# Optimization experiments

Hardware: AMD Instinct MI355X
Metric: run time of the kernel (lower is better)

The kernel has to match this reference:

```python
import jax, jax.numpy as jnp
import numpy as np

N_NODES = 100000
N_EDGES = 1600000
IN_DIM = 29
OUT_DIM = 64
BN_EPS = 1e-5


def setup_inputs() -> dict:
    key = jax.random.key(0)
    k1, k2, k3, k4, k5, k6, k7, k8 = jax.random.split(key, 8)
    node = jax.random.normal(k1, (N_NODES, 3), dtype=jnp.float32)
    features = jax.random.normal(k2, (N_NODES, IN_DIM), dtype=jnp.float32)
    edges = jax.random.randint(k3, (N_EDGES, 2), 0, N_NODES, dtype=jnp.int64)
    # Linear(input_dim+3, output_dim, bias=False): weight [out, in+3]
    fan_in = IN_DIM + 3
    weight = jax.random.uniform(k4, (OUT_DIM, fan_in), dtype=jnp.float32,
                                minval=-1.0, maxval=1.0) / np.sqrt(fan_in)
    # BatchNorm1d(output_dim) in eval mode: affine params + running stats
    gamma = jax.random.normal(k5, (OUT_DIM,), dtype=jnp.float32) * 0.1 + 1.0
    beta = jax.random.normal(k6, (OUT_DIM,), dtype=jnp.float32) * 0.1
    running_mean = jax.random.normal(k7, (OUT_DIM,), dtype=jnp.float32) * 0.1
    running_var = jax.random.uniform(k8, (OUT_DIM,), dtype=jnp.float32,
                                     minval=0.5, maxval=1.5)
    return {"node": node, "features": features, "edges": edges,
            "weight": weight, "gamma": gamma, "beta": beta,
            "running_mean": running_mean, "running_var": running_var}


def reference(node, features, edges, weight, gamma, beta, running_mean, running_var):
    dst = edges[:, 0]  # pos_i index (pooling destination)
    src = edges[:, 1]  # pos_j / x_j index
    # gather + concat: msg [E, in+3]
    msg = jnp.concatenate([features[src], node[src] - node[dst]], axis=1)
    # Linear (no bias): [E, out]
    msg = jnp.einsum('ei,oi->eo', msg, weight)
    # BatchNorm1d (eval mode, running stats)
    inv_std = gamma / jnp.sqrt(running_var + BN_EPS)
    msg = (msg - running_mean) * inv_std + beta
    # scatter-max pooling over destination nodes (fixed N segments;
    # torch.unique + scatter_reduce(amax) == segment_max restricted to covered
    # nodes; empty segments filled with 0 matching the zeros init)
    pooled = jax.ops.segment_max(msg, dst, num_segments=N_NODES)
    return jnp.where(jnp.isneginf(pooled), 0.0, pooled)
```

## Files before the change

### kernel.cpp

```cpp
#include <hip/hip_runtime.h>
#include <hip/hip_fp16.h>

#define IN_DIM 29
#define XDIM 32
#define OUT_DIM 64
#define BN_EPS 1e-5f

#define BW      32
#define BW_LOG  5
#define PBLK    256
#define TBLK    2048
#define MAXBUCK 4096
#define SENT    0

#define CS_BPB  32
#define CS_SEG  32

typedef float float4u __attribute__((ext_vector_type(4), aligned(4)));


__global__ __launch_bounds__(256) void fused_tc_kernel(
    const float* __restrict__ features, const float* __restrict__ node,
    const float* __restrict__ weight, const float* __restrict__ gamma,
    const float* __restrict__ rvar, unsigned short* __restrict__ yq,
    const int* __restrict__ edges, int* __restrict__ gHist,
    int n_nodes, int npw, int n_edges, int nbuck, int chunk_c, int cblk)
{
    if ((int)blockIdx.x < cblk) {
        __shared__ int h[MAXBUCK];
        for (int i = threadIdx.x; i < nbuck; i += 256) h[i] = 0;
        __syncthreads();
        const int e0 = blockIdx.x * chunk_c;
        const int e1 = min(e0 + chunk_c, n_edges);
        for (int e = e0 + threadIdx.x; e < e1; e += 256)
            atomicAdd(&h[edges[2*e] >> BW_LOG], 1);
        __syncthreads();
        int* row = gHist + (size_t)blockIdx.x * nbuck;
        for (int i = threadIdx.x; i < nbuck; i += 256) row[i] = h[i];
    } else {
        const int lane = threadIdx.x & 63;
        const int wave = (((int)blockIdx.x - cblk) * 256 + (int)threadIdx.x) >> 6;
        int n0 = wave * npw;
        int n1 = n0 + npw; if (n1 > n_nodes) n1 = n_nodes;

        float w[XDIM];
        const float4* wp = (const float4*)(weight + lane * XDIM);
#pragma unroll
        for (int q = 0; q < 8; ++q) {
            float4 v = wp[q];
            w[4*q+0] = v.x; w[4*q+1] = v.y; w[4*q+2] = v.z; w[4*q+3] = v.w;
        }
        const float a = gamma[lane] * __frsqrt_rn(rvar[lane] + BN_EPS);

        for (int n = n0; n < n1; ++n) {
            const float* f = features + (size_t)n * IN_DIM;
            const float4u* f4 = (const float4u*)f;
            float x[XDIM];
#pragma unroll
            for (int q = 0; q < 7; ++q) {
                float4u v = f4[q];
                x[4*q+0] = v.x; x[4*q+1] = v.y; x[4*q+2] = v.z; x[4*q+3] = v.w;
            }
            x[28] = f[28];
            const float* nd = node + (size_t)n * 3;
            x[29] = nd[0]; x[30] = nd[1]; x[31] = nd[2];
            float acc = 0.0f;
#pragma unroll
            for (int i = 0; i < XDIM; ++i) acc = fmaf(x[i], w[i], acc);
            unsigned short hh = __half_as_ushort(__float2half(acc * a));
            unsigned short enc = (hh & 0x8000) ? (unsigned short)(~hh)
                                               : (unsigned short)(hh | 0x8000);
            yq[(size_t)n * OUT_DIM + lane] = enc;
        }
    }
}

__global__ __launch_bounds__(1024) void colscan_kernel(
    int* __restrict__ gHist, int* __restrict__ bTot,
    int nbuck, int cblk, int R)
{
    const int il = threadIdx.x & (CS_BPB - 1);
    const int s  = threadIdx.x / CS_BPB;
    const int i  = blockIdx.x * CS_BPB + il;
    const int rows = cblk / CS_SEG;
    const int j0 = s * rows;
    __shared__ int sums[CS_SEG][CS_BPB + 1];

    int total = 0;
    if (i < nbuck) {
#pragma unroll 4
        for (int r = 0; r < rows; ++r)
            total += gHist[(size_t)(j0 + r) * nbuck + i];
    }
    sums[s][il] = total;
    __syncthreads();
    if (s == 0) {
        int run = 0;
#pragma unroll
        for (int k = 0; k < CS_SEG; ++k) {
            int t = sums[k][il]; sums[k][il] = run; run += t;
        }
        if (i < nbuck) bTot[i] = run;
    }
    __syncthreads();
    if (i < nbuck) {
        int run = sums[s][il];
        for (int g = j0; g < j0 + rows; g += R) {
            int t[4];
            for (int r = 0; r < R; ++r) t[r] = gHist[(size_t)(g + r) * nbuck + i];
            gHist[(size_t)g * nbuck + i] = run;
            for (int r = 0; r < R; ++r) run += t[r];
        }
    }
}

__global__ __launch_bounds__(256) void scan_b_kernel(int* __restrict__ aux, int nb) {
    const int t = threadIdx.x;
    const int lane = t & 63, wv = t >> 6;
    __shared__ int wsum[4];
    __shared__ int s_run;
    if (t == 0) s_run = 0;
    __syncthreads();
    for (int base = 0; base < nb; base += 256) {
        const int i = base + t;
        int v = (i < nb) ? aux[i] : 0;
        int x = v;
#pragma unroll
        for (int off = 1; off < 64; off <<= 1) {
            int y = __shfl_up(x, off);
            if (lane >= off) x += y;
        }
        if (lane == 63) wsum[wv] = x;
        __syncthreads();
        int wexcl = 0;
        for (int k = 0; k < wv; ++k) wexcl += wsum[k];
        const int run = s_run;
        if (i < nb) aux[i] = run + wexcl + x - v;
        __syncthreads();
        if (t == 255) s_run = run + wexcl + x;
        __syncthreads();
    }
}

__global__ __launch_bounds__(1024) void partition_kernel(
    const int* __restrict__ edges, const int* __restrict__ gHist,
    const int* __restrict__ bOffs,
    int* __restrict__ keys, int n_edges, int nbuck, int chunk_c, int R)
{
    __shared__ int cur[MAXBUCK];
    const int* prow = gHist + (size_t)(R * blockIdx.x) * nbuck;
    for (int i = threadIdx.x; i < nbuck; i += 1024)
        cur[i] = prow[i] + bOffs[i];
    __syncthreads();
    const int chunk_p = R * chunk_c;
    const int e0 = blockIdx.x * chunk_p;
    const int e1 = min(e0 + chunk_p, n_edges);
    for (int e = e0 + threadIdx.x; e < e1; e += 1024) {
        const int dst = edges[2*e], src = edges[2*e+1];
        const int b = dst >> BW_LOG;
        const int pos = atomicAdd(&cur[b], 1);
        keys[pos] = (dst & (BW - 1)) | (src << BW_LOG);
    }
}

__global__ __launch_bounds__(256) void pool_fused_kernel(
    const int* __restrict__ bOffs, const int* __restrict__ keys,
    const unsigned short* __restrict__ yq, const float* __restrict__ node,
    const float* __restrict__ weight, const float* __restrict__ gamma,
    const float* __restrict__ beta, const float* __restrict__ rmean,
    const float* __restrict__ rvar,
    float* __restrict__ out, int n_nodes, int n_edges, int nbuck)
{
    __shared__ int acc[BW * OUT_DIM];
    const int tid = threadIdx.x;
    const int lane = tid & 63, wid = tid >> 6;
    const int b = blockIdx.x;

    {
        int4* p = (int4*)acc;
        for (int i = tid; i < BW * OUT_DIM / 4; i += 256)
            p[i] = make_int4(SENT, SENT, SENT, SENT);
    }
    __syncthreads();

    const int beg = bOffs[b];
    const int end = (b == nbuck - 1) ? n_edges : bOffs[b + 1];

    const int cnt = end - beg;
    const int slice = (cnt + 3) >> 2;
    const int w_beg = beg + wid * slice;
    const int w_end = min(w_beg + slice, end);

    if (w_beg < w_end) {
        const int last = w_end - 1;
        int j = w_beg;
        int kv = keys[min(j + lane, last)];
        while (j < w_end) {
            const int jn = j + 64;
            int kv_n = 0;
            if (jn < w_end) kv_n = keys[min(jn + lane, last)];
            const int m = w_end - j < 64 ? w_end - j : 64;
            const int ng = (m + 7) >> 3;

            unsigned int va[8]; int da[8];
#pragma unroll
            for (int u = 0; u < 8; ++u) {
                const int uu = (u < m) ? u : (m - 1);
                const int key = __builtin_amdgcn_readlane(kv, uu);
                da[u] = key & (BW - 1);
                va[u] = yq[(size_t)((unsigned)key >> BW_LOG) * OUT_DIM + lane];
            }
            for (int g = 0; g < ng; ++g) {
                unsigned int vb[8]; int db[8];
                const bool more = (g + 1 < ng);
                if (more) {
#pragma unroll
                    for (int u = 0; u < 8; ++u) {
                        int uu = (g + 1) * 8 + u; uu = (uu < m) ? uu : (m - 1);
                        const int key = __builtin_amdgcn_readlane(kv, uu);
                        db[u] = key & (BW - 1);
                        vb[u] = yq[(size_t)((unsigned)key >> BW_LOG) * OUT_DIM + lane];
                    }
                }
#pragma unroll
                for (int u = 0; u < 8; ++u)
                    atomicMax(&acc[da[u] * OUT_DIM + lane], (int)va[u]);
                if (more) {
#pragma unroll
                    for (int u = 0; u < 8; ++u) { va[u] = vb[u]; da[u] = db[u]; }
                }
            }
            j = jn; kv = kv_n;
        }
    }
    __syncthreads();

    const float a  = gamma[lane] * __frsqrt_rn(rvar[lane] + BN_EPS);
    const float bp = beta[lane] - rmean[lane] * a;
    const float w29 = weight[lane * XDIM + 29] * a;
    const float w30 = weight[lane * XDIM + 30] * a;
    const float w31 = weight[lane * XDIM + 31] * a;

    for (int d = wid; d < BW; d += 4) {
        const int dg = b * BW + d;
        if (dg >= n_nodes) break;
        const int k = acc[d * OUT_DIM + lane];
        float rr;
        if (k == SENT) {
            rr = 0.0f;
        } else {
            const unsigned short enc = (unsigned short)k;
            const unsigned short h = (enc & 0x8000) ? (unsigned short)(enc ^ 0x8000)
                                                    : (unsigned short)(~enc);
            const float v = __half2float(__ushort_as_half(h));
            const float nx = node[(size_t)dg * 3 + 0];
            const float ny = node[(size_t)dg * 3 + 1];
            const float nz = node[(size_t)dg * 3 + 2];
            rr = v + (bp - (w29 * nx + w30 * ny + w31 * nz));
        }
        out[(size_t)dg * OUT_DIM + lane] = rr;
    }
}

__global__ void init_kernel(int4* __restrict__ out, int total4) {
    int t = blockIdx.x * blockDim.x + threadIdx.x;
    if (t < total4) out[t] = make_int4(INT_MIN, INT_MIN, INT_MIN, INT_MIN);
}

__global__ __launch_bounds__(256) void edge_atomic_kernel(
    const int* __restrict__ edges,
    const float* __restrict__ features, const float* __restrict__ node,
    const float* __restrict__ weight, const float* __restrict__ gamma,
    const float* __restrict__ beta, const float* __restrict__ rmean,
    const float* __restrict__ rvar,
    int* __restrict__ out, int n_edges, int epw)
{
    const int lane = threadIdx.x & 63;
    const int wave = (blockIdx.x * blockDim.x + threadIdx.x) >> 6;
    int e0 = wave * epw, e1 = e0 + epw;
    if (e1 > n_edges) e1 = n_edges;

    float w[XDIM];
    const float4* wp = (const float4*)(weight + lane * XDIM);
#pragma unroll
    for (int q = 0; q < 8; ++q) {
        float4 v = wp[q];
        w[4*q+0] = v.x; w[4*q+1] = v.y; w[4*q+2] = v.z; w[4*q+3] = v.w;
    }
    const float a = gamma[lane] * __frsqrt_rn(rvar[lane] + BN_EPS);
    const float bprime = beta[lane] - rmean[lane] * a;

    for (int e = e0; e < e1; ++e) {
        const int dst = edges[2*e+0], src = edges[2*e+1];
        float x[XDIM];
#pragma unroll
        for (int i = 0; i < IN_DIM; ++i) x[i] = features[(size_t)src * IN_DIM + i];
#pragma unroll
        for (int j = 0; j < 3; ++j)
            x[IN_DIM+j] = node[(size_t)src*3+j] - node[(size_t)dst*3+j];
        float acc = 0.0f;
#pragma unroll
        for (int i = 0; i < XDIM; ++i) acc = fmaf(x[i], w[i], acc);
        float msg = fmaf(acc, a, bprime);
        int bb = __float_as_int(msg);
        int key = (bb < 0) ? (bb ^ 0x7FFFFFFF) : bb;
        atomicMax(out + (size_t)dst * OUT_DIM + lane, key);
    }
}

__global__ void decode_kernel(int* __restrict__ out, int total) {
    int t = blockIdx.x * blockDim.x + threadIdx.x;
    if (t >= total) return;
    int k = out[t];
    float r;
    if (k == INT_MIN) r = 0.0f;
    else { int b = (k < 0) ? (k ^ 0x7FFFFFFF) : k; r = __int_as_float(b); }
    ((float*)out)[t] = r;
}

extern "C" void kernel_launch(void* const* d_in, const int* in_sizes, int n_in,
                              void* d_out, int out_size, void* d_ws, size_t ws_size,
                              hipStream_t stream) {
    const float* node     = (const float*)d_in[0];
    const float* features = (const float*)d_in[1];
    const int*   edges    = (const int*)d_in[2];
    const float* weight   = (const float*)d_in[3];
    const float* gamma    = (const float*)d_in[4];
    const float* beta     = (const float*)d_in[5];
    const float* rmean    = (const float*)d_in[6];
    const float* rvar     = (const float*)d_in[7];

    const int n_nodes = in_sizes[0] / 3;
    const int n_edges = in_sizes[2] / 2;

    const int nbuck = (n_nodes + BW - 1) >> BW_LOG;

    int cblk = 0; size_t o_yq=0, o_hist=0, o_boffs=0, o_keys=0;
    for (int cand = 512; cand >= 128; cand >>= 1) {
        size_t off = 0;
        auto alloc = [&](size_t bytes) { size_t r = off; off = (off + bytes + 15) & ~(size_t)15; return r; };
        o_yq    = alloc((size_t)n_nodes * OUT_DIM * sizeof(unsigned short));
        o_hist  = alloc((size_t)cand * nbuck * sizeof(int));
        o_boffs = alloc((size_t)nbuck * sizeof(int));
        o_keys  = alloc((size_t)n_edges * sizeof(int));
        if (off <= ws_size) { cblk = cand; break; }
    }

    if (cblk > 0 && nbuck <= MAXBUCK && n_nodes <= MAXBUCK * BW) {
        const int pblk = (cblk < PBLK) ? cblk : PBLK;
        const int R = cblk / pblk;
        const int chunk_c = (n_edges + cblk - 1) / cblk;
        const int npw = (n_nodes + TBLK * 4 - 1) / (TBLK * 4);

        char* base  = (char*)d_ws;
        unsigned short* yq = (unsigned short*)(base + o_yq);
        int* gHist  = (int*)(base + o_hist);
        int* bOffs  = (int*)(base + o_boffs);
        int* keys   = (int*)(base + o_keys);

        fused_tc_kernel<<<cblk + TBLK, 256, 0, stream>>>(
            features, node, weight, gamma, rvar, yq,
            edges, gHist, n_nodes, npw, n_edges, nbuck, chunk_c, cblk);
        colscan_kernel<<<(nbuck + CS_BPB - 1) / CS_BPB, 1024, 0, stream>>>(
            gHist, bOffs, nbuck, cblk, R);
        scan_b_kernel<<<1, 256, 0, stream>>>(bOffs, nbuck);
        partition_kernel<<<pblk, 1024, 0, stream>>>(
            edges, gHist, bOffs, keys, n_edges, nbuck, chunk_c, R);
        pool_fused_kernel<<<nbuck, 256, 0, stream>>>(
            bOffs, keys, yq, node, weight, gamma, beta, rmean, rvar,
            (float*)d_out, n_nodes, n_edges, nbuck);
    } else {
        int* out_i = (int*)d_out;
        const int total4 = out_size / 4;
        init_kernel<<<(total4 + 255) / 256, 256, 0, stream>>>((int4*)out_i, total4);
        const int n_waves = 8192;
        const int epw = (n_edges + n_waves - 1) / n_waves;
        edge_atomic_kernel<<<n_waves / 4, 256, 0, stream>>>(
            edges, features, node, weight, gamma, beta, rmean, rvar,
            out_i, n_edges, epw);
        decode_kernel<<<(out_size + 255) / 256, 256, 0, stream>>>(out_i, out_size);
    }
}
```

Before: 204.8 us.

## Split fused transform/histogram kernel and prefetch node rows with finer work split

Splits the combined node-transform and edge-histogram kernel into two separate launches. The transform now gives each wave 4 nodes (more blocks) and software-prefetches the next node's features, while the histogram kernel reads edges as int2 with 4-way unrolled loads. The partition block count is also halved. This aims to improve latency hiding and load balance, at the cost of an extra launch and losing the overlap between the two halves.

Measured after the change: 217.3 us. +6.1%, slower.

```diff
diff --git a/kernel.cpp b/kernel.cpp
--- a/kernel.cpp
+++ b/kernel.cpp
@@ -8,8 +8,7 @@
 
 #define BW      32
 #define BW_LOG  5
-#define PBLK    256
-#define TBLK    2048
+#define PBLK    128
 #define MAXBUCK 4096
 #define SENT    0
 
@@ -19,60 +18,94 @@
 typedef float float4u __attribute__((ext_vector_type(4), aligned(4)));
 
 
-__global__ __launch_bounds__(256) void fused_tc_kernel(
+__global__ __launch_bounds__(256) void transform_kernel(
     const float* __restrict__ features, const float* __restrict__ node,
     const float* __restrict__ weight, const float* __restrict__ gamma,
     const float* __restrict__ rvar, unsigned short* __restrict__ yq,
-    const int* __restrict__ edges, int* __restrict__ gHist,
-    int n_nodes, int npw, int n_edges, int nbuck, int chunk_c, int cblk)
-{
-    if ((int)blockIdx.x < cblk) {
-        __shared__ int h[MAXBUCK];
-        for (int i = threadIdx.x; i < nbuck; i += 256) h[i] = 0;
-        __syncthreads();
-        const int e0 = blockIdx.x * chunk_c;
-        const int e1 = min(e0 + chunk_c, n_edges);
-        for (int e = e0 + threadIdx.x; e < e1; e += 256)
-            atomicAdd(&h[edges[2*e] >> BW_LOG], 1);
-        __syncthreads();
-        int* row = gHist + (size_t)blockIdx.x * nbuck;
-        for (int i = threadIdx.x; i < nbuck; i += 256) row[i] = h[i];
-    } else {
-        const int lane = threadIdx.x & 63;
-        const int wave = (((int)blockIdx.x - cblk) * 256 + (int)threadIdx.x) >> 6;
-        int n0 = wave * npw;
-        int n1 = n0 + npw; if (n1 > n_nodes) n1 = n_nodes;
-
-        float w[XDIM];
-        const float4* wp = (const float4*)(weight + lane * XDIM);
-#pragma unroll
-        for (int q = 0; q < 8; ++q) {
-            float4 v = wp[q];
-            w[4*q+0] = v.x; w[4*q+1] = v.y; w[4*q+2] = v.z; w[4*q+3] = v.w;
-        }
-        const float a = gamma[lane] * __frsqrt_rn(rvar[lane] + BN_EPS);
-
-        for (int n = n0; n < n1; ++n) {
-            const float* f = features + (size_t)n * IN_DIM;
+    int n_nodes, int npw)
+{
+    const int lane = threadIdx.x & 63;
+    const int wave = (blockIdx.x * 256 + (int)threadIdx.x) >> 6;
+    const int n0 = wave * npw;
+    const int n1 = min(n0 + npw, n_nodes);
+    if (n0 >= n1) return;
+
+    float w[XDIM];
+    const float4* wp = (const float4*)(weight + lane * XDIM);
+#pragma unroll
+    for (int q = 0; q < 8; ++q) {
+        float4 v = wp[q];
+        w[4*q+0] = v.x; w[4*q+1] = v.y; w[4*q+2] = v.z; w[4*q+3] = v.w;
+    }
+    const float a = gamma[lane] * __frsqrt_rn(rvar[lane] + BN_EPS);
+
+    float x[XDIM];
+    {
+        const float* f = features + (size_t)n0 * IN_DIM;
+        const float4u* f4 = (const float4u*)f;
+#pragma unroll
+        for (int q = 0; q < 7; ++q) {
+            float4u v = f4[q];
+            x[4*q+0] = v.x; x[4*q+1] = v.y; x[4*q+2] = v.z; x[4*q+3] = v.w;
+        }
+        x[28] = f[28];
+        const float* nd = node + (size_t)n0 * 3;
+        x[29] = nd[0]; x[30] = nd[1]; x[31] = nd[2];
+    }
+
+    for (int n = n0; n < n1; ++n) {
+        float xn[XDIM];
+        if (n + 1 < n1) {
+            const float* f = features + (size_t)(n + 1) * IN_DIM;
             const float4u* f4 = (const float4u*)f;
-            float x[XDIM];
 #pragma unroll
             for (int q = 0; q < 7; ++q) {
                 float4u v = f4[q];
-                x[4*q+0] = v.x; x[4*q+1] = v.y; x[4*q+2] = v.z; x[4*q+3] = v.w;
+                xn[4*q+0] = v.x; xn[4*q+1] = v.y; xn[4*q+2] = v.z; xn[4*q+3] = v.w;
             }
-            x[28] = f[28];
-            const float* nd = node + (size_t)n * 3;
-            x[29] = nd[0]; x[30] = nd[1]; x[31] = nd[2];
-            float acc = 0.0f;
-#pragma unroll
-            for (int i = 0; i < XDIM; ++i) acc = fmaf(x[i], w[i], acc);
-            unsigned short hh = __half_as_ushort(__float2half(acc * a));
-            unsigned short enc = (hh & 0x8000) ? (unsigned short)(~hh)
-                                               : (unsigned short)(hh | 0x8000);
-            yq[(size_t)n * OUT_DIM + lane] = enc;
-        }
-    }
+            xn[28] = f[28];
+            const float* nd = node + (size_t)(n + 1) * 3;
+            xn[29] = nd[0]; xn[30] = nd[1]; xn[31] = nd[2];
+        }
+        float acc = 0.0f;
+#pragma unroll
+        for (int i = 0; i < XDIM; ++i) acc = fmaf(x[i], w[i], acc);
+        unsigned short hh = __half_as_ushort(__float2half(acc * a));
+        unsigned short enc = (hh & 0x8000) ? (unsigned short)(~hh)
+                                           : (unsigned short)(hh | 0x8000);
+        yq[(size_t)n * OUT_DIM + lane] = enc;
+        if (n + 1 < n1) {
+#pragma unroll
+            for (int i = 0; i < XDIM; ++i) x[i] = xn[i];
+        }
+    }
+}
+
+__global__ __launch_bounds__(256) void count_kernel(
+    const int2* __restrict__ edges2, int* __restrict__ gHist,
+    int n_edges, int nbuck, int chunk_c)
+{
+    __shared__ int h[MAXBUCK];
+    for (int i = threadIdx.x; i < nbuck; i += 256) h[i] = 0;
+    __syncthreads();
+    const int e0 = blockIdx.x * chunk_c;
+    const int e1 = min(e0 + chunk_c, n_edges);
+    int e = e0 + threadIdx.x;
+    for (; e + 3 * 256 < e1; e += 4 * 256) {
+        int d0 = edges2[e          ].x;
+        int d1 = edges2[e +     256].x;
+        int d2 = edges2[e + 2 * 256].x;
+        int d3 = edges2[e + 3 * 256].x;
+        atomicAdd(&h[d0 >> BW_LOG], 1);
+        atomicAdd(&h[d1 >> BW_LOG], 1);
+        atomicAdd(&h[d2 >> BW_LOG], 1);
+        atomicAdd(&h[d3 >> BW_LOG], 1);
+    }
+    for (; e < e1; e += 256)
+        atomicAdd(&h[edges2[e].x >> BW_LOG], 1);
+    __syncthreads();
+    int* row = gHist + (size_t)blockIdx.x * nbuck;
+    for (int i = threadIdx.x; i < nbuck; i += 256) row[i] = h[i];
 }
 
 __global__ __launch_bounds__(1024) void colscan_kernel(
@@ -350,7 +383,9 @@
         const int pblk = (cblk < PBLK) ? cblk : PBLK;
         const int R = cblk / pblk;
         const int chunk_c = (n_edges + cblk - 1) / cblk;
-        const int npw = (n_nodes + TBLK * 4 - 1) / (TBLK * 4);
+        const int npw = 4;
+        const int t_waves = (n_nodes + npw - 1) / npw;
+        const int t_blocks = (t_waves + 3) / 4;
 
         char* base  = (char*)d_ws;
         unsigned short* yq = (unsigned short*)(base + o_yq);
@@ -358,9 +393,10 @@
         int* bOffs  = (int*)(base + o_boffs);
         int* keys   = (int*)(base + o_keys);
 
-        fused_tc_kernel<<<cblk + TBLK, 256, 0, stream>>>(
-            features, node, weight, gamma, rvar, yq,
-            edges, gHist, n_nodes, npw, n_edges, nbuck, chunk_c, cblk);
+        transform_kernel<<<t_blocks, 256, 0, stream>>>(
+            features, node, weight, gamma, rvar, yq, n_nodes, npw);
+        count_kernel<<<cblk, 256, 0, stream>>>(
+            (const int2*)edges, gHist, n_edges, nbuck, chunk_c);
         colscan_kernel<<<(nbuck + CS_BPB - 1) / CS_BPB, 1024, 0, stream>>>(
             gHist, bOffs, nbuck, cblk, R);
         scan_b_kernel<<<1, 256, 0, stream>>>(bOffs, nbuck);
```
